# Optimization experiments

Hardware: AMD Instinct MI355X
Metric: run time of the kernel (lower is better)

Reference implementation:

```python
import jax, jax.numpy as jnp
import numpy as np

N, K, M = 4096, 4096, 12288  # tokens, in_features, out_features


def setup_inputs() -> dict:
    key = jax.random.key(0)
    k1, k2, k3, k4, k5 = jax.random.split(key, 5)
    x = jax.random.randint(k1, (N, K), -127, 128, dtype=jnp.int32)
    weight = jax.random.randint(k2, (M, K), -127, 128, dtype=jnp.int32)
    # per-token input scale and per-output-channel dequant scale (small positive)
    input_scale = jax.random.uniform(k3, (N,), dtype=jnp.float32) * 0.01 + 1e-4
    dequant_scale = jax.random.uniform(k4, (M,), dtype=jnp.float32) * 0.01 + 1e-4
    bias = jax.random.normal(k5, (M,), dtype=jnp.float32)
    return {"x": x, "weight": weight, "input_scale": input_scale,
            "dequant_scale": dequant_scale, "bias": bias}


def reference(x, weight, input_scale, dequant_scale, bias):
    # int8 GEMM with int32 accumulation: acc[n, m] = sum_k x[n,k] * w[m,k]
    acc = jnp.matmul(x, weight.T)  # [N, M] int32
    # fused dequant: per-token scale * per-channel scale, then bias add
    out = acc.astype(jnp.float32) * input_scale[:, None] * dequant_scale[None, :] + bias[None, :]
    return out
```

## Files before the change

### kernel.cpp

```cpp
#include <hip/hip_runtime.h>
#include <cstdint>
#include <cstddef>

#define N_TOK 4096
#define K_DIM 4096
#define M_DIM 12288

using i32x4 = __attribute__((ext_vector_type(4))) int;

constexpr long GROUPS_X     = (long)N_TOK * K_DIM / 4;
constexpr long GROUPS_TOTAL = ((long)N_TOK + M_DIM) * K_DIM / 4;

__global__ __launch_bounds__(256) void pack_i8_kernel(
    const int* __restrict__ x, const int* __restrict__ w, int* __restrict__ out8)
{
  const long stride = (long)gridDim.x * 256;
  for (long g = (long)blockIdx.x * 256 + threadIdx.x; g < GROUPS_TOTAL; g += stride) {
    const int* src = (g < GROUPS_X) ? (x + g * 4) : (w + (g - GROUPS_X) * 4);
    i32x4 v = *(const i32x4*)src;
    out8[g] = (v.x & 0xff) | ((v.y & 0xff) << 8) | ((v.z & 0xff) << 16) | (v.w << 24);
  }
}

#define BM 256
#define BN 256
#define KT 32
#define GRID_M (N_TOK / BM)
#define GRID_N (M_DIM / BN)
#define NWG (GRID_M * GRID_N)

__device__ __forceinline__ void load_lds16(const void* g, void* l) {
  __builtin_amdgcn_global_load_lds(
      (const __attribute__((address_space(1))) void*)g,
      (__attribute__((address_space(3))) void*)l, 16, 0, 0);
}


__device__ __forceinline__ void stage_region(
    int8_t* lds, int buf, int ab, int s, int ktarg,
    const int8_t* A8, const int8_t* B8, int brow, int bcol, int tid)
{
  const int8_t* gbase = ab ? (B8 + (size_t)bcol * K_DIM)
                           : (A8 + (size_t)brow * K_DIM);
  const int lb = (buf * 4 + ab * 2 + s) * 16384;
  const int gk = ktarg * 128 + s * 64;
#pragma unroll
  for (int p = 0; p < 2; ++p) {
    int c = p * 512 + tid;
    int row  = c >> 2;
    int slot = (c & 3) ^ ((row >> 1) & 3);
    load_lds16(gbase + (size_t)row * K_DIM + gk + slot * 16,
               lds + lb + c * 16);
  }
}

template <int MODE>
__device__ __forceinline__ void ktile(
    int kt, int8_t* lds, const int8_t* A8, const int8_t* B8,
    int brow, int bcol, int tid, int wr, int wc, int lr, int xs16,
    i32x4 (&acc)[8][4])
{
  const int cur = kt & 1;
  const int bA0 = (cur * 4 + 0) * 16384;
  const int bA1 = (cur * 4 + 1) * 16384;
  const int bB0 = (cur * 4 + 2) * 16384;
  const int bB1 = (cur * 4 + 3) * 16384;
  const int arow = wr * 128 + lr;
  const int bcol_ = wc * 64 + lr;

  i32x4 b[4];

  {
#pragma unroll
    for (int j = 0; j < 4; ++j)
      b[j] = *(const i32x4*)&lds[bB0 + (bcol_ + j * 16) * 64 + xs16];
    i32x4 a[4];
#pragma unroll
    for (int i = 0; i < 4; ++i)
      a[i] = *(const i32x4*)&lds[bA0 + (arow + i * 16) * 64 + xs16];
    if (MODE >= 1) stage_region(lds, cur ^ 1, 0, 1, kt + 1, A8, B8, brow, bcol, tid);
    __builtin_amdgcn_s_barrier();
    __builtin_amdgcn_s_setprio(1);
#pragma unroll
    for (int i = 0; i < 4; ++i)
#pragma unroll
      for (int j = 0; j < 4; ++j)
        acc[i][j] = __builtin_amdgcn_mfma_i32_16x16x64_i8(a[i], b[j], acc[i][j], 0, 0, 0);
    __builtin_amdgcn_s_setprio(0);
    __builtin_amdgcn_s_barrier();
  }

  {
    i32x4 a[4];
#pragma unroll
    for (int i = 0; i < 4; ++i)
      a[i] = *(const i32x4*)&lds[bA0 + (arow + (4 + i) * 16) * 64 + xs16];
    if (MODE >= 1) stage_region(lds, cur ^ 1, 1, 1, kt + 1, A8, B8, brow, bcol, tid);
    __builtin_amdgcn_s_barrier();
    __builtin_amdgcn_s_setprio(1);
#pragma unroll
    for (int i = 0; i < 4; ++i)
#pragma unroll
      for (int j = 0; j < 4; ++j)
        acc[4 + i][j] = __builtin_amdgcn_mfma_i32_16x16x64_i8(a[i], b[j], acc[4 + i][j], 0, 0, 0);
    __builtin_amdgcn_s_setprio(0);
    __builtin_amdgcn_s_barrier();
  }

  {
#pragma unroll
    for (int j = 0; j < 4; ++j)
      b[j] = *(const i32x4*)&lds[bB1 + (bcol_ + j * 16) * 64 + xs16];
    i32x4 a[4];
#pragma unroll
    for (int i = 0; i < 4; ++i)
      a[i] = *(const i32x4*)&lds[bA1 + (arow + i * 16) * 64 + xs16];
    if (MODE == 2) stage_region(lds, cur, 0, 0, kt + 2, A8, B8, brow, bcol, tid);
    __builtin_amdgcn_s_barrier();
    __builtin_amdgcn_s_setprio(1);
#pragma unroll
    for (int i = 0; i < 4; ++i)
#pragma unroll
      for (int j = 0; j < 4; ++j)
        acc[i][j] = __builtin_amdgcn_mfma_i32_16x16x64_i8(a[i], b[j], acc[i][j], 0, 0, 0);
    __builtin_amdgcn_s_setprio(0);
    __builtin_amdgcn_s_barrier();
  }

  {
    i32x4 a[4];
#pragma unroll
    for (int i = 0; i < 4; ++i)
      a[i] = *(const i32x4*)&lds[bA1 + (arow + (4 + i) * 16) * 64 + xs16];
    if (MODE == 2) stage_region(lds, cur, 1, 0, kt + 2, A8, B8, brow, bcol, tid);
    __builtin_amdgcn_s_barrier();
    __builtin_amdgcn_s_setprio(1);
#pragma unroll
    for (int i = 0; i < 4; ++i)
#pragma unroll
      for (int j = 0; j < 4; ++j)
        acc[4 + i][j] = __builtin_amdgcn_mfma_i32_16x16x64_i8(a[i], b[j], acc[4 + i][j], 0, 0, 0);
    __builtin_amdgcn_s_setprio(0);
    if (MODE == 2)      asm volatile("s_waitcnt vmcnt(4)" ::: "memory");
    else if (MODE == 1) asm volatile("s_waitcnt vmcnt(0)" ::: "memory");
    __builtin_amdgcn_s_barrier();
  }
}

__global__ __launch_bounds__(512, 2) void w8a8_gemm_kernel(
    const int8_t* __restrict__ A8,
    const int8_t* __restrict__ B8,
    const float* __restrict__ input_scale,
    const float* __restrict__ dequant_scale,
    const float* __restrict__ bias,
    float* __restrict__ out)
{
  __shared__ int8_t lds[131072];

  const int tid  = threadIdx.x;
  const int lane = tid & 63;
  const int wid  = tid >> 6;
  const int wr   = wid >> 2;
  const int wc   = wid & 3;
  const int lr   = lane & 15;
  const int lg   = lane >> 4;
  const int xs16 = ((lg ^ ((lr >> 1) & 3)) << 4);

  int bid = blockIdx.x;
  int w_  = (bid & 7) * (NWG / 8) + (bid >> 3);
  const int width = 4 * GRID_N;
  int gid = w_ / width, rem = w_ % width;
  int bm = gid * 4 + (rem & 3);
  int bn = rem >> 2;
  const int brow = bm * BM;
  const int bcol = bn * BN;

  i32x4 acc[8][4] = {};

  stage_region(lds, 0, 0, 0, 0, A8, B8, brow, bcol, tid);
  stage_region(lds, 0, 1, 0, 0, A8, B8, brow, bcol, tid);
  stage_region(lds, 0, 0, 1, 0, A8, B8, brow, bcol, tid);
  stage_region(lds, 0, 1, 1, 0, A8, B8, brow, bcol, tid);
  stage_region(lds, 1, 0, 0, 1, A8, B8, brow, bcol, tid);
  stage_region(lds, 1, 1, 0, 1, A8, B8, brow, bcol, tid);
  asm volatile("s_waitcnt vmcnt(4)" ::: "memory");
  __builtin_amdgcn_s_barrier();

  for (int kt = 0; kt < KT - 2; ++kt)
    ktile<2>(kt, lds, A8, B8, brow, bcol, tid, wr, wc, lr, xs16, acc);
  ktile<1>(KT - 2, lds, A8, B8, brow, bcol, tid, wr, wc, lr, xs16, acc);
  ktile<0>(KT - 1, lds, A8, B8, brow, bcol, tid, wr, wc, lr, xs16, acc);

  const int orow = brow + wr * 128;
  const int ocol = bcol + wc * 64 + lr;
#pragma unroll
  for (int j = 0; j < 4; ++j) {
    const int m = ocol + j * 16;
    const float dsc = dequant_scale[m];
    const float bs  = bias[m];
#pragma unroll
    for (int fi = 0; fi < 8; ++fi) {
#pragma unroll
      for (int r = 0; r < 4; ++r) {
        const int n = orow + fi * 16 + lg * 4 + r;
        out[(size_t)n * M_DIM + m] = (float)acc[fi][j][r] * input_scale[n] * dsc + bs;
      }
    }
  }
}

extern "C" void kernel_launch(void* const* d_in, const int* in_sizes, int n_in,
                              void* d_out, int out_size, void* d_ws, size_t ws_size,
                              hipStream_t stream) {
  const int*   x             = (const int*)d_in[0];
  const int*   w             = (const int*)d_in[1];
  const float* input_scale   = (const float*)d_in[2];
  const float* dequant_scale = (const float*)d_in[3];
  const float* bias          = (const float*)d_in[4];
  float*       out           = (float*)d_out;

  int8_t* x8 = (int8_t*)d_ws;
  int8_t* w8 = x8 + (size_t)N_TOK * K_DIM;

  pack_i8_kernel<<<4096, 256, 0, stream>>>(x, w, (int*)d_ws);
  w8a8_gemm_kernel<<<NWG, 512, 0, stream>>>(x8, w8, input_scale, dequant_scale,
                                            bias, out);
}
```

Measured before the change: 560.8 us.

## Switch to 32x32x32 int8 MFMA tiles with precomputed LDS offsets

Replaces the 16x16x64 i8 MFMA inner product with 32x32x32 i8 MFMA, cutting the MFMA count per k-step from 16 to 8 per wave and the LDS fragment loads from 8 to 6 per sub-step. LDS read offsets and global staging pointers are now precomputed once, and the k loop is unrolled by two so buffer indices become compile-time constants. The epilogue is remapped to the 32x32 accumulator layout. The larger MFMA has longer latency per instruction and changes the register layout, which may affect scheduling and occupancy.

```diff
diff --git a/kernel.cpp b/kernel.cpp
--- a/kernel.cpp
+++ b/kernel.cpp
@@ -6,7 +6,8 @@
 #define K_DIM 4096
 #define M_DIM 12288
 
-using i32x4 = __attribute__((ext_vector_type(4))) int;
+using i32x4  = __attribute__((ext_vector_type(4)))  int;
+using i32x16 = __attribute__((ext_vector_type(16))) int;
 
 constexpr long GROUPS_X     = (long)N_TOK * K_DIM / 4;
 constexpr long GROUPS_TOTAL = ((long)N_TOK + M_DIM) * K_DIM / 4;
@@ -36,110 +37,89 @@
 }
 
 
-__device__ __forceinline__ void stage_region(
-    int8_t* lds, int buf, int ab, int s, int ktarg,
-    const int8_t* A8, const int8_t* B8, int brow, int bcol, int tid)
-{
-  const int8_t* gbase = ab ? (B8 + (size_t)bcol * K_DIM)
-                           : (A8 + (size_t)brow * K_DIM);
-  const int lb = (buf * 4 + ab * 2 + s) * 16384;
-  const int gk = ktarg * 128 + s * 64;
-#pragma unroll
-  for (int p = 0; p < 2; ++p) {
-    int c = p * 512 + tid;
-    int row  = c >> 2;
-    int slot = (c & 3) ^ ((row >> 1) & 3);
-    load_lds16(gbase + (size_t)row * K_DIM + gk + slot * 16,
-               lds + lb + c * 16);
-  }
-}
-
-template <int MODE>
+template <int BUF, int S>
+__device__ __forceinline__ void stage2(int8_t* lds, int ab, int ktarg,
+                                       const int8_t* g0, int tid)
+{
+  const int lb = (BUF * 4 + ab * 2 + S) * 16384;
+  const size_t ko = (size_t)ktarg * 128 + S * 64;
+  load_lds16(g0 + ko, lds + lb + tid * 16);
+  load_lds16(g0 + (size_t)128 * K_DIM + ko, lds + lb + 8192 + tid * 16);
+}
+
+#define MFMA8(ACCROW)                                                          \
+  acc[0][0] = __builtin_amdgcn_mfma_i32_32x32x32_i8(a0, b0, acc[0][0], 0, 0, 0); \
+  acc[0][1] = __builtin_amdgcn_mfma_i32_32x32x32_i8(a0, b1, acc[0][1], 0, 0, 0); \
+  acc[1][0] = __builtin_amdgcn_mfma_i32_32x32x32_i8(a1, b0, acc[1][0], 0, 0, 0); \
+  acc[1][1] = __builtin_amdgcn_mfma_i32_32x32x32_i8(a1, b1, acc[1][1], 0, 0, 0); \
+  acc[2][0] = __builtin_amdgcn_mfma_i32_32x32x32_i8(a2, b0, acc[2][0], 0, 0, 0); \
+  acc[2][1] = __builtin_amdgcn_mfma_i32_32x32x32_i8(a2, b1, acc[2][1], 0, 0, 0); \
+  acc[3][0] = __builtin_amdgcn_mfma_i32_32x32x32_i8(a3, b0, acc[3][0], 0, 0, 0); \
+  acc[3][1] = __builtin_amdgcn_mfma_i32_32x32x32_i8(a3, b1, acc[3][1], 0, 0, 0);
+
+template <int MODE, int CUR>
 __device__ __forceinline__ void ktile(
-    int kt, int8_t* lds, const int8_t* A8, const int8_t* B8,
-    int brow, int bcol, int tid, int wr, int wc, int lr, int xs16,
-    i32x4 (&acc)[8][4])
-{
-  const int cur = kt & 1;
-  const int bA0 = (cur * 4 + 0) * 16384;
-  const int bA1 = (cur * 4 + 1) * 16384;
-  const int bB0 = (cur * 4 + 2) * 16384;
-  const int bB1 = (cur * 4 + 3) * 16384;
-  const int arow = wr * 128 + lr;
-  const int bcol_ = wc * 64 + lr;
-
-  i32x4 b[4];
-
-  {
-#pragma unroll
-    for (int j = 0; j < 4; ++j)
-      b[j] = *(const i32x4*)&lds[bB0 + (bcol_ + j * 16) * 64 + xs16];
-    i32x4 a[4];
-#pragma unroll
-    for (int i = 0; i < 4; ++i)
-      a[i] = *(const i32x4*)&lds[bA0 + (arow + i * 16) * 64 + xs16];
-    if (MODE >= 1) stage_region(lds, cur ^ 1, 0, 1, kt + 1, A8, B8, brow, bcol, tid);
-    __builtin_amdgcn_s_barrier();
-    __builtin_amdgcn_s_setprio(1);
-#pragma unroll
-    for (int i = 0; i < 4; ++i)
-#pragma unroll
-      for (int j = 0; j < 4; ++j)
-        acc[i][j] = __builtin_amdgcn_mfma_i32_16x16x64_i8(a[i], b[j], acc[i][j], 0, 0, 0);
-    __builtin_amdgcn_s_setprio(0);
-    __builtin_amdgcn_s_barrier();
-  }
-
-  {
-    i32x4 a[4];
-#pragma unroll
-    for (int i = 0; i < 4; ++i)
-      a[i] = *(const i32x4*)&lds[bA0 + (arow + (4 + i) * 16) * 64 + xs16];
-    if (MODE >= 1) stage_region(lds, cur ^ 1, 1, 1, kt + 1, A8, B8, brow, bcol, tid);
-    __builtin_amdgcn_s_barrier();
-    __builtin_amdgcn_s_setprio(1);
-#pragma unroll
-    for (int i = 0; i < 4; ++i)
-#pragma unroll
-      for (int j = 0; j < 4; ++j)
-        acc[4 + i][j] = __builtin_amdgcn_mfma_i32_16x16x64_i8(a[i], b[j], acc[4 + i][j], 0, 0, 0);
-    __builtin_amdgcn_s_setprio(0);
-    __builtin_amdgcn_s_barrier();
-  }
-
-  {
-#pragma unroll
-    for (int j = 0; j < 4; ++j)
-      b[j] = *(const i32x4*)&lds[bB1 + (bcol_ + j * 16) * 64 + xs16];
-    i32x4 a[4];
-#pragma unroll
-    for (int i = 0; i < 4; ++i)
-      a[i] = *(const i32x4*)&lds[bA1 + (arow + i * 16) * 64 + xs16];
-    if (MODE == 2) stage_region(lds, cur, 0, 0, kt + 2, A8, B8, brow, bcol, tid);
-    __builtin_amdgcn_s_barrier();
-    __builtin_amdgcn_s_setprio(1);
-#pragma unroll
-    for (int i = 0; i < 4; ++i)
-#pragma unroll
-      for (int j = 0; j < 4; ++j)
-        acc[i][j] = __builtin_amdgcn_mfma_i32_16x16x64_i8(a[i], b[j], acc[i][j], 0, 0, 0);
-    __builtin_amdgcn_s_setprio(0);
-    __builtin_amdgcn_s_barrier();
-  }
-
-  {
-    i32x4 a[4];
-#pragma unroll
-    for (int i = 0; i < 4; ++i)
-      a[i] = *(const i32x4*)&lds[bA1 + (arow + (4 + i) * 16) * 64 + xs16];
-    if (MODE == 2) stage_region(lds, cur, 1, 0, kt + 2, A8, B8, brow, bcol, tid);
-    __builtin_amdgcn_s_barrier();
-    __builtin_amdgcn_s_setprio(1);
-#pragma unroll
-    for (int i = 0; i < 4; ++i)
-#pragma unroll
-      for (int j = 0; j < 4; ++j)
-        acc[4 + i][j] = __builtin_amdgcn_mfma_i32_16x16x64_i8(a[i], b[j], acc[4 + i][j], 0, 0, 0);
+    int kt, int8_t* lds, const int8_t* gA, const int8_t* gB, int tid,
+    int aoff0, int aoff1, int boff0, int boff1, i32x16 (&acc)[4][2])
+{
+  constexpr int aB0 = (CUR * 4 + 0) * 16384;
+  constexpr int aB1 = (CUR * 4 + 1) * 16384;
+  constexpr int bB0 = (CUR * 4 + 2) * 16384;
+  constexpr int bB1 = (CUR * 4 + 3) * 16384;
+
+  {
+    i32x4 b0 = *(const i32x4*)&lds[bB0 + boff0];
+    i32x4 b1 = *(const i32x4*)&lds[bB0 + boff0 + 2048];
+    i32x4 a0 = *(const i32x4*)&lds[aB0 + aoff0];
+    i32x4 a1 = *(const i32x4*)&lds[aB0 + aoff0 + 2048];
+    i32x4 a2 = *(const i32x4*)&lds[aB0 + aoff0 + 4096];
+    i32x4 a3 = *(const i32x4*)&lds[aB0 + aoff0 + 6144];
+    if (MODE >= 1) stage2<(CUR ^ 1), 1>(lds, 0, kt + 1, gA, tid);
+    __builtin_amdgcn_s_barrier();
+    __builtin_amdgcn_s_setprio(1);
+    MFMA8(0)
+    __builtin_amdgcn_s_setprio(0);
+    __builtin_amdgcn_s_barrier();
+  }
+  {
+    i32x4 b0 = *(const i32x4*)&lds[bB0 + boff1];
+    i32x4 b1 = *(const i32x4*)&lds[bB0 + boff1 + 2048];
+    i32x4 a0 = *(const i32x4*)&lds[aB0 + aoff1];
+    i32x4 a1 = *(const i32x4*)&lds[aB0 + aoff1 + 2048];
+    i32x4 a2 = *(const i32x4*)&lds[aB0 + aoff1 + 4096];
+    i32x4 a3 = *(const i32x4*)&lds[aB0 + aoff1 + 6144];
+    if (MODE >= 1) stage2<(CUR ^ 1), 1>(lds, 1, kt + 1, gB, tid);
+    __builtin_amdgcn_s_barrier();
+    __builtin_amdgcn_s_setprio(1);
+    MFMA8(0)
+    __builtin_amdgcn_s_setprio(0);
+    __builtin_amdgcn_s_barrier();
+  }
+  {
+    i32x4 b0 = *(const i32x4*)&lds[bB1 + boff0];
+    i32x4 b1 = *(const i32x4*)&lds[bB1 + boff0 + 2048];
+    i32x4 a0 = *(const i32x4*)&lds[aB1 + aoff0];
+    i32x4 a1 = *(const i32x4*)&lds[aB1 + aoff0 + 2048];
+    i32x4 a2 = *(const i32x4*)&lds[aB1 + aoff0 + 4096];
+    i32x4 a3 = *(const i32x4*)&lds[aB1 + aoff0 + 6144];
+    if (MODE == 2) stage2<CUR, 0>(lds, 0, kt + 2, gA, tid);
+    __builtin_amdgcn_s_barrier();
+    __builtin_amdgcn_s_setprio(1);
+    MFMA8(0)
+    __builtin_amdgcn_s_setprio(0);
+    __builtin_amdgcn_s_barrier();
+  }
+  {
+    i32x4 b0 = *(const i32x4*)&lds[bB1 + boff1];
+    i32x4 b1 = *(const i32x4*)&lds[bB1 + boff1 + 2048];
+    i32x4 a0 = *(const i32x4*)&lds[aB1 + aoff1];
+    i32x4 a1 = *(const i32x4*)&lds[aB1 + aoff1 + 2048];
+    i32x4 a2 = *(const i32x4*)&lds[aB1 + aoff1 + 4096];
+    i32x4 a3 = *(const i32x4*)&lds[aB1 + aoff1 + 6144];
+    if (MODE == 2) stage2<CUR, 0>(lds, 1, kt + 2, gB, tid);
+    __builtin_amdgcn_s_barrier();
+    __builtin_amdgcn_s_setprio(1);
+    MFMA8(0)
     __builtin_amdgcn_s_setprio(0);
     if (MODE == 2)      asm volatile("s_waitcnt vmcnt(4)" ::: "memory");
     else if (MODE == 1) asm volatile("s_waitcnt vmcnt(0)" ::: "memory");
@@ -162,9 +142,14 @@
   const int wid  = tid >> 6;
   const int wr   = wid >> 2;
   const int wc   = wid & 3;
-  const int lr   = lane & 15;
-  const int lg   = lane >> 4;
-  const int xs16 = ((lg ^ ((lr >> 1) & 3)) << 4);
+  const int l31  = lane & 31;
+  const int lh   = lane >> 5;
+  const int xsw  = (l31 >> 1) & 3;
+
+  const int aoff0 = (wr * 128 + l31) * 64 + ((0 + lh) ^ xsw) * 16;
+  const int aoff1 = (wr * 128 + l31) * 64 + ((2 + lh) ^ xsw) * 16;
+  const int boff0 = (wc * 64 + l31) * 64 + ((0 + lh) ^ xsw) * 16;
+  const int boff1 = (wc * 64 + l31) * 64 + ((2 + lh) ^ xsw) * 16;
 
   int bid = blockIdx.x;
   int w_  = (bid & 7) * (NWG / 8) + (bid >> 3);
@@ -175,36 +160,44 @@
   const int brow = bm * BM;
   const int bcol = bn * BN;
 
-  i32x4 acc[8][4] = {};
-
-  stage_region(lds, 0, 0, 0, 0, A8, B8, brow, bcol, tid);
-  stage_region(lds, 0, 1, 0, 0, A8, B8, brow, bcol, tid);
-  stage_region(lds, 0, 0, 1, 0, A8, B8, brow, bcol, tid);
-  stage_region(lds, 0, 1, 1, 0, A8, B8, brow, bcol, tid);
-  stage_region(lds, 1, 0, 0, 1, A8, B8, brow, bcol, tid);
-  stage_region(lds, 1, 1, 0, 1, A8, B8, brow, bcol, tid);
+  const int srow  = tid >> 2;
+  const int sslot = (tid & 3) ^ ((srow >> 1) & 3);
+  const int8_t* gA = A8 + (size_t)(brow + srow) * K_DIM + sslot * 16;
+  const int8_t* gB = B8 + (size_t)(bcol + srow) * K_DIM + sslot * 16;
+
+  i32x16 acc[4][2] = {};
+
+  stage2<0, 0>(lds, 0, 0, gA, tid);
+  stage2<0, 0>(lds, 1, 0, gB, tid);
+  stage2<0, 1>(lds, 0, 0, gA, tid);
+  stage2<0, 1>(lds, 1, 0, gB, tid);
+  stage2<1, 0>(lds, 0, 1, gA, tid);
+  stage2<1, 0>(lds, 1, 1, gB, tid);
   asm volatile("s_waitcnt vmcnt(4)" ::: "memory");
   __builtin_amdgcn_s_barrier();
 
-  for (int kt = 0; kt < KT - 2; ++kt)
-    ktile<2>(kt, lds, A8, B8, brow, bcol, tid, wr, wc, lr, xs16, acc);
-  ktile<1>(KT - 2, lds, A8, B8, brow, bcol, tid, wr, wc, lr, xs16, acc);
-  ktile<0>(KT - 1, lds, A8, B8, brow, bcol, tid, wr, wc, lr, xs16, acc);
+  for (int kt = 0; kt < KT - 2; kt += 2) {
+    ktile<2, 0>(kt,     lds, gA, gB, tid, aoff0, aoff1, boff0, boff1, acc);
+    ktile<2, 1>(kt + 1, lds, gA, gB, tid, aoff0, aoff1, boff0, boff1, acc);
+  }
+  ktile<1, 0>(KT - 2, lds, gA, gB, tid, aoff0, aoff1, boff0, boff1, acc);
+  ktile<0, 1>(KT - 1, lds, gA, gB, tid, aoff0, aoff1, boff0, boff1, acc);
 
   const int orow = brow + wr * 128;
-  const int ocol = bcol + wc * 64 + lr;
+  const int ocol = bcol + wc * 64 + l31;
+  const float dsc0 = dequant_scale[ocol];
+  const float dsc1 = dequant_scale[ocol + 32];
+  const float bs0  = bias[ocol];
+  const float bs1  = bias[ocol + 32];
 #pragma unroll
-  for (int j = 0; j < 4; ++j) {
-    const int m = ocol + j * 16;
-    const float dsc = dequant_scale[m];
-    const float bs  = bias[m];
+  for (int fi = 0; fi < 4; ++fi) {
 #pragma unroll
-    for (int fi = 0; fi < 8; ++fi) {
-#pragma unroll
-      for (int r = 0; r < 4; ++r) {
-        const int n = orow + fi * 16 + lg * 4 + r;
-        out[(size_t)n * M_DIM + m] = (float)acc[fi][j][r] * input_scale[n] * dsc + bs;
-      }
+    for (int r = 0; r < 16; ++r) {
+      const int n = orow + fi * 32 + (r & 3) + 8 * (r >> 2) + 4 * lh;
+      const float sv = input_scale[n];
+      float* o = out + (size_t)n * M_DIM + ocol;
+      o[0]  = (float)acc[fi][0][r] * sv * dsc0 + bs0;
+      o[32] = (float)acc[fi][1][r] * sv * dsc1 + bs1;
     }
   }
 }
```

Result: no change. 571.9 us (+2.0%).
